# Kernel tuning notes

Hardware: AMD Instinct MI355X
Metric: run time of the kernel (lower is better)

The kernel has to match this reference:

```python
import jax, jax.numpy as jnp
import numpy as np


def setup_inputs() -> dict:
    key = jax.random.key(0)
    kq, kk, kv = jax.random.split(key, 3)
    n, d = 8192, 32
    return {
        "Q": jax.random.normal(kq, (n, d), dtype=jnp.float32),
        "K": jax.random.normal(kk, (n, d), dtype=jnp.float32),
        "V": jax.random.normal(kv, (n, d), dtype=jnp.float32),
    }


def reference(Q, K, V):
    # FlashAttention-2 tiling with online softmax is mathematically equivalent
    # to full (unscaled, unmasked) softmax attention: O = softmax(Q K^T) V.
    # Note: the original module applies NO 1/sqrt(d) scaling.
    S = jnp.einsum("qd,kd->qk", Q, K)           # [n, n]
    P = jax.nn.softmax(S, axis=-1)                # numerically stable softmax
    return jnp.einsum("qk,kd->qd", P, V)         # [n, d]
```

## Files before the change

kernel.cpp:

```cpp
#include <hip/hip_runtime.h>
#include <hip/hip_bf16.h>

typedef __bf16 bf16x8 __attribute__((ext_vector_type(8)));
typedef __bf16 bf16x4 __attribute__((ext_vector_type(4)));
typedef float  f32x4  __attribute__((ext_vector_type(4)));
typedef unsigned short u16;

static constexpr int N = 8192;
static constexpr int D = 32;
static constexpr float L2E = 1.44269504088896340736f;
static constexpr float MSHIFT = 32.0f;

__global__ __launch_bounds__(256) void prep_kernel(
    const float* __restrict__ Q, const float* __restrict__ K,
    const float* __restrict__ V, u16* __restrict__ Qb, u16* __restrict__ Kb,
    u16* __restrict__ Vt) {
  const int b = blockIdx.x;
  auto pack = [](float x, float y) -> unsigned int {
    u16 ux = __builtin_bit_cast(u16, (__bf16)x);
    u16 uy = __builtin_bit_cast(u16, (__bf16)y);
    return (unsigned int)ux | ((unsigned int)uy << 16);
  };
  if (b < 256) {
    const int i = (b * 256 + threadIdx.x) * 4;
    const float4 q = *reinterpret_cast<const float4*>(Q + i);
    const float4 k = *reinterpret_cast<const float4*>(K + i);
    uint2 qo = { pack(q.x * L2E, q.y * L2E), pack(q.z * L2E, q.w * L2E) };
    uint2 ko = { pack(k.x, k.y), pack(k.z, k.w) };
    *reinterpret_cast<uint2*>(Qb + i) = qo;
    *reinterpret_cast<uint2*>(Kb + i) = ko;
  } else {
    const int r = (b - 256) * 256 + threadIdx.x;
    float vr[32];
#pragma unroll
    for (int j = 0; j < 8; ++j) {
      const float4 v = *reinterpret_cast<const float4*>(V + r * D + j * 4);
      vr[4 * j] = v.x; vr[4 * j + 1] = v.y; vr[4 * j + 2] = v.z; vr[4 * j + 3] = v.w;
    }
#pragma unroll
    for (int d = 0; d < 32; ++d)
      Vt[d * N + r] = __builtin_bit_cast(u16, (__bf16)vr[d]);
  }
}

__global__ __launch_bounds__(512, 4) void flash_kernel(
    const u16* __restrict__ Qb, const u16* __restrict__ Kb,
    const u16* __restrict__ Vt, float* __restrict__ lP,
    float* __restrict__ OP, int kpb) {
  __shared__ u16 Ks[2][64 * 32];
  __shared__ u16 Vs[2][32 * 64];

  const int tid = threadIdx.x;
  const int lane = tid & 63;
  const int wave = tid >> 6;
  const int a = lane & 15;
  const int g = lane >> 4;
  const int qg = blockIdx.x & 31;
  const int sp = blockIdx.x >> 5;
  const int qr0 = qg * 256 + wave * 32;
  const int k0 = sp * kpb;
  const int nt = kpb >> 6;

  const bf16x8 qfA = *reinterpret_cast<const bf16x8*>(Qb + (qr0 + a) * D + g * 8);
  const bf16x8 qfB = *reinterpret_cast<const bf16x8*>(Qb + (qr0 + 16 + a) * D + g * 8);

  const int krow = tid >> 3;
  const int ks8 = tid & 7;
  const int kl8 = (((ks8 >> 1) ^ ((krow >> 1) & 3)) << 1) | (ks8 & 1);
  const int vd = tid >> 4;
  const int vps = tid & 15;
  const int vls = vps ^ (vd & 15);
  const u16* __restrict__ ksrc = Kb + krow * D + kl8 * 4;
  const u16* __restrict__ vsrc = Vt + (size_t)vd * N + vls * 4;

  const f32x4 zero4 = {0.f, 0.f, 0.f, 0.f};
  const f32x4 minit = {-MSHIFT, -MSHIFT, -MSHIFT, -MSHIFT};
  f32x4 accA0 = zero4, accA1 = zero4, accB0 = zero4, accB1 = zero4;
  float lA = 0.f, lB = 0.f;

  uint2 kreg = *reinterpret_cast<const uint2*>(ksrc + (size_t)k0 * D);
  uint2 vreg = *reinterpret_cast<const uint2*>(vsrc + k0);
  *reinterpret_cast<uint2*>(&Ks[0][(size_t)tid * 4]) = kreg;
  *reinterpret_cast<uint2*>(&Vs[0][(size_t)tid * 4]) = vreg;
  if (nt > 1) {
    kreg = *reinterpret_cast<const uint2*>(ksrc + (size_t)(k0 + 64) * D);
    vreg = *reinterpret_cast<const uint2*>(vsrc + k0 + 64);
  }
  __syncthreads();

  for (int t = 0; t < nt; ++t) {
    const int cur = t & 1;
    const int nxt = cur ^ 1;
    if (t + 1 < nt) {
      *reinterpret_cast<uint2*>(&Ks[nxt][(size_t)tid * 4]) = kreg;
      *reinterpret_cast<uint2*>(&Vs[nxt][(size_t)tid * 4]) = vreg;
    }
    if (t + 2 < nt) {
      kreg = *reinterpret_cast<const uint2*>(ksrc + (size_t)(k0 + (t + 2) * 64) * D);
      vreg = *reinterpret_cast<const uint2*>(vsrc + k0 + (t + 2) * 64);
    }

    bf16x8 kf[4];
#pragma unroll
    for (int t4 = 0; t4 < 4; ++t4) {
      const int row = 16 * t4 + a;
      kf[t4] = *reinterpret_cast<const bf16x8*>(
          &Ks[cur][row * 32 + ((g ^ ((a >> 1) & 3)) << 3)]);
    }
    bf16x4 v0[4], v1[4];
#pragma unroll
    for (int tt = 0; tt < 4; ++tt) {
      const int slot = ((g + 4 * tt) ^ a) << 2;
      v0[tt] = *reinterpret_cast<const bf16x4*>(&Vs[cur][a * 64 + slot]);
      v1[tt] = *reinterpret_cast<const bf16x4*>(&Vs[cur][(16 + a) * 64 + slot]);
    }

    f32x4 sA[4], sB[4];
#pragma unroll
    for (int t4 = 0; t4 < 4; ++t4) {
      sA[t4] = __builtin_amdgcn_mfma_f32_16x16x32_bf16(kf[t4], qfA, minit, 0, 0, 0);
      sB[t4] = __builtin_amdgcn_mfma_f32_16x16x32_bf16(kf[t4], qfB, minit, 0, 0, 0);
    }

    float pA[4][4], pB[4][4];
#pragma unroll
    for (int t4 = 0; t4 < 4; ++t4) {
#pragma unroll
      for (int r = 0; r < 4; ++r) {
        pA[t4][r] = __builtin_amdgcn_exp2f(sA[t4][r]);
        pB[t4][r] = __builtin_amdgcn_exp2f(sB[t4][r]);
        lA += pA[t4][r];
        lB += pB[t4][r];
      }
    }

    const bf16x8 pfA0 = {(__bf16)pA[0][0], (__bf16)pA[0][1], (__bf16)pA[0][2], (__bf16)pA[0][3],
                         (__bf16)pA[1][0], (__bf16)pA[1][1], (__bf16)pA[1][2], (__bf16)pA[1][3]};
    const bf16x8 pfA1 = {(__bf16)pA[2][0], (__bf16)pA[2][1], (__bf16)pA[2][2], (__bf16)pA[2][3],
                         (__bf16)pA[3][0], (__bf16)pA[3][1], (__bf16)pA[3][2], (__bf16)pA[3][3]};
    const bf16x8 pfB0 = {(__bf16)pB[0][0], (__bf16)pB[0][1], (__bf16)pB[0][2], (__bf16)pB[0][3],
                         (__bf16)pB[1][0], (__bf16)pB[1][1], (__bf16)pB[1][2], (__bf16)pB[1][3]};
    const bf16x8 pfB1 = {(__bf16)pB[2][0], (__bf16)pB[2][1], (__bf16)pB[2][2], (__bf16)pB[2][3],
                         (__bf16)pB[3][0], (__bf16)pB[3][1], (__bf16)pB[3][2], (__bf16)pB[3][3]};

    const bf16x8 va00 = __builtin_shufflevector(v0[0], v0[1], 0, 1, 2, 3, 4, 5, 6, 7);
    const bf16x8 va01 = __builtin_shufflevector(v0[2], v0[3], 0, 1, 2, 3, 4, 5, 6, 7);
    const bf16x8 va10 = __builtin_shufflevector(v1[0], v1[1], 0, 1, 2, 3, 4, 5, 6, 7);
    const bf16x8 va11 = __builtin_shufflevector(v1[2], v1[3], 0, 1, 2, 3, 4, 5, 6, 7);

    accA0 = __builtin_amdgcn_mfma_f32_16x16x32_bf16(va00, pfA0, accA0, 0, 0, 0);
    accA1 = __builtin_amdgcn_mfma_f32_16x16x32_bf16(va10, pfA0, accA1, 0, 0, 0);
    accB0 = __builtin_amdgcn_mfma_f32_16x16x32_bf16(va00, pfB0, accB0, 0, 0, 0);
    accB1 = __builtin_amdgcn_mfma_f32_16x16x32_bf16(va10, pfB0, accB1, 0, 0, 0);
    accA0 = __builtin_amdgcn_mfma_f32_16x16x32_bf16(va01, pfA1, accA0, 0, 0, 0);
    accA1 = __builtin_amdgcn_mfma_f32_16x16x32_bf16(va11, pfA1, accA1, 0, 0, 0);
    accB0 = __builtin_amdgcn_mfma_f32_16x16x32_bf16(va01, pfB1, accB0, 0, 0, 0);
    accB1 = __builtin_amdgcn_mfma_f32_16x16x32_bf16(va11, pfB1, accB1, 0, 0, 0);

    __syncthreads();
  }

  lA += __shfl_xor(lA, 16, 64);
  lA += __shfl_xor(lA, 32, 64);
  lB += __shfl_xor(lB, 16, 64);
  lB += __shfl_xor(lB, 32, 64);

  float* obA = OP + (size_t)(sp * N + qr0 + a) * D;
  float* obB = OP + (size_t)(sp * N + qr0 + 16 + a) * D;
#pragma unroll
  for (int r = 0; r < 4; ++r) {
    obA[4 * g + r] = accA0[r];
    obA[16 + 4 * g + r] = accA1[r];
    obB[4 * g + r] = accB0[r];
    obB[16 + 4 * g + r] = accB1[r];
  }
  if (g == 0) {
    lP[sp * N + qr0 + a] = lA;
    lP[sp * N + qr0 + 16 + a] = lB;
  }
}

template <int NS>
__global__ __launch_bounds__(256) void combine_kernel(
    const float* __restrict__ lP, const float* __restrict__ OP,
    float* __restrict__ out) {
  const int idx = blockIdx.x * 256 + threadIdx.x;
  if (idx >= N * D) return;
  const int q = idx >> 5;
  float L = 0.f, o = 0.f;
#pragma unroll
  for (int s = 0; s < NS; ++s) {
    L += lP[s * N + q];
    o += OP[(size_t)s * N * D + idx];
  }
  out[idx] = o / L;
}

extern "C" void kernel_launch(void* const* d_in, const int* in_sizes, int n_in,
                              void* d_out, int out_size, void* d_ws, size_t ws_size,
                              hipStream_t stream) {
  const float* Q = (const float*)d_in[0];
  const float* K = (const float*)d_in[1];
  const float* V = (const float*)d_in[2];
  float* out = (float*)d_out;

  const size_t base = (size_t)3 * N * D * sizeof(u16);
  const size_t per_split = (size_t)N * sizeof(float) + (size_t)N * D * sizeof(float);
  int ns = 16;
  while (ns > 4 && base + (size_t)ns * per_split > ws_size) ns >>= 1;

  u16* Qb = (u16*)d_ws;
  u16* Kb = Qb + N * D;
  u16* Vt = Kb + N * D;
  float* lP = (float*)(Vt + N * D);
  float* OP = lP + ns * N;

  prep_kernel<<<256 + N / 256, 256, 0, stream>>>(Q, K, V, Qb, Kb, Vt);
  flash_kernel<<<32 * ns, 512, 0, stream>>>(Qb, Kb, Vt, lP, OP, N / ns);
  switch (ns) {
    case 16: combine_kernel<16><<<(N * D) / 256, 256, 0, stream>>>(lP, OP, out); break;
    case 8:  combine_kernel<8><<<(N * D) / 256, 256, 0, stream>>>(lP, OP, out); break;
    default: combine_kernel<4><<<(N * D) / 256, 256, 0, stream>>>(lP, OP, out); break;
  }
}
```

Baseline: 36.03 us.

## Transpose V through LDS and use 128-query blocks with 16-byte tile loads

The V transpose in the prep kernel now stages a 64-row tile in shared memory, so each thread writes a packed 16-byte row of Vt. Previously each thread issued scattered 2-byte global stores. The flash kernel shrinks from 512 to 256 threads per block, covering 128 queries, and launches twice as many blocks. K/V tiles are loaded with 16-byte loads, using a swizzle and half-swap that keep the existing LDS read pattern valid. Scheduling barriers pin the prefetch order; in exchange, each K/V tile is reused by fewer waves, which adds LDS fill traffic per query.

```diff
diff --git a/kernel.cpp b/kernel.cpp
--- a/kernel.cpp
+++ b/kernel.cpp
@@ -15,6 +15,7 @@
     const float* __restrict__ Q, const float* __restrict__ K,
     const float* __restrict__ V, u16* __restrict__ Qb, u16* __restrict__ Kb,
     u16* __restrict__ Vt) {
+  __shared__ float tile[64][33];
   const int b = blockIdx.x;
   auto pack = [](float x, float y) -> unsigned int {
     u16 ux = __builtin_bit_cast(u16, (__bf16)x);
@@ -30,20 +31,28 @@
     *reinterpret_cast<uint2*>(Qb + i) = qo;
     *reinterpret_cast<uint2*>(Kb + i) = ko;
   } else {
-    const int r = (b - 256) * 256 + threadIdx.x;
-    float vr[32];
-#pragma unroll
-    for (int j = 0; j < 8; ++j) {
-      const float4 v = *reinterpret_cast<const float4*>(V + r * D + j * 4);
-      vr[4 * j] = v.x; vr[4 * j + 1] = v.y; vr[4 * j + 2] = v.z; vr[4 * j + 3] = v.w;
-    }
-#pragma unroll
-    for (int d = 0; d < 32; ++d)
-      Vt[d * N + r] = __builtin_bit_cast(u16, (__bf16)vr[d]);
-  }
-}
-
-__global__ __launch_bounds__(512, 4) void flash_kernel(
+    const int r0 = (b - 256) * 64;
+    const int row = threadIdx.x >> 2;
+    const int c0 = (threadIdx.x & 3) * 8;
+    const float4 x0 = *reinterpret_cast<const float4*>(V + (size_t)(r0 + row) * D + c0);
+    const float4 x1 = *reinterpret_cast<const float4*>(V + (size_t)(r0 + row) * D + c0 + 4);
+    tile[row][c0 + 0] = x0.x; tile[row][c0 + 1] = x0.y;
+    tile[row][c0 + 2] = x0.z; tile[row][c0 + 3] = x0.w;
+    tile[row][c0 + 4] = x1.x; tile[row][c0 + 5] = x1.y;
+    tile[row][c0 + 6] = x1.z; tile[row][c0 + 7] = x1.w;
+    __syncthreads();
+    const int d = threadIdx.x >> 3;
+    const int kc = (threadIdx.x & 7) * 8;
+    uint4 o;
+    o.x = pack(tile[kc + 0][d], tile[kc + 1][d]);
+    o.y = pack(tile[kc + 2][d], tile[kc + 3][d]);
+    o.z = pack(tile[kc + 4][d], tile[kc + 5][d]);
+    o.w = pack(tile[kc + 6][d], tile[kc + 7][d]);
+    *reinterpret_cast<uint4*>(Vt + (size_t)d * N + r0 + kc) = o;
+  }
+}
+
+__global__ __launch_bounds__(256, 4) void flash_kernel(
     const u16* __restrict__ Qb, const u16* __restrict__ Kb,
     const u16* __restrict__ Vt, float* __restrict__ lP,
     float* __restrict__ OP, int kpb) {
@@ -55,36 +64,40 @@
   const int wave = tid >> 6;
   const int a = lane & 15;
   const int g = lane >> 4;
-  const int qg = blockIdx.x & 31;
-  const int sp = blockIdx.x >> 5;
-  const int qr0 = qg * 256 + wave * 32;
+  const int qg = blockIdx.x & 63;
+  const int sp = blockIdx.x >> 6;
+  const int qr0 = qg * 128 + wave * 32;
   const int k0 = sp * kpb;
   const int nt = kpb >> 6;
 
   const bf16x8 qfA = *reinterpret_cast<const bf16x8*>(Qb + (qr0 + a) * D + g * 8);
   const bf16x8 qfB = *reinterpret_cast<const bf16x8*>(Qb + (qr0 + 16 + a) * D + g * 8);
 
-  const int krow = tid >> 3;
-  const int ks8 = tid & 7;
-  const int kl8 = (((ks8 >> 1) ^ ((krow >> 1) & 3)) << 1) | (ks8 & 1);
-  const int vd = tid >> 4;
-  const int vps = tid & 15;
-  const int vls = vps ^ (vd & 15);
-  const u16* __restrict__ ksrc = Kb + krow * D + kl8 * 4;
-  const u16* __restrict__ vsrc = Vt + (size_t)vd * N + vls * 4;
-
+  const int krow = tid >> 2;
+  const int kslot = (tid & 3) ^ ((krow >> 1) & 3);
+  const u16* __restrict__ ksrc = Kb + krow * D + kslot * 8;
+  const int vd = tid >> 3;
+  const int v16 = tid & 7;
+  const int vblk = v16 ^ ((vd >> 1) & 7);
+  const bool vswap = (vd & 1) != 0;
+  const u16* __restrict__ vsrc = Vt + (size_t)vd * N + vblk * 8;
+
+  const f32x4 minit = {-MSHIFT, -MSHIFT, -MSHIFT, -MSHIFT};
   const f32x4 zero4 = {0.f, 0.f, 0.f, 0.f};
-  const f32x4 minit = {-MSHIFT, -MSHIFT, -MSHIFT, -MSHIFT};
   f32x4 accA0 = zero4, accA1 = zero4, accB0 = zero4, accB1 = zero4;
   float lA = 0.f, lB = 0.f;
 
-  uint2 kreg = *reinterpret_cast<const uint2*>(ksrc + (size_t)k0 * D);
-  uint2 vreg = *reinterpret_cast<const uint2*>(vsrc + k0);
-  *reinterpret_cast<uint2*>(&Ks[0][(size_t)tid * 4]) = kreg;
-  *reinterpret_cast<uint2*>(&Vs[0][(size_t)tid * 4]) = vreg;
+  {
+    const uint4 kr = *reinterpret_cast<const uint4*>(ksrc + (size_t)k0 * D);
+    const uint4 vr = *reinterpret_cast<const uint4*>(vsrc + k0);
+    const uint4 vw = vswap ? uint4{vr.z, vr.w, vr.x, vr.y} : vr;
+    *reinterpret_cast<uint4*>(&Ks[0][(size_t)tid * 8]) = kr;
+    *reinterpret_cast<uint4*>(&Vs[0][(size_t)tid * 8]) = vw;
+  }
+  uint4 kreg = {0, 0, 0, 0}, vreg = {0, 0, 0, 0};
   if (nt > 1) {
-    kreg = *reinterpret_cast<const uint2*>(ksrc + (size_t)(k0 + 64) * D);
-    vreg = *reinterpret_cast<const uint2*>(vsrc + k0 + 64);
+    kreg = *reinterpret_cast<const uint4*>(ksrc + (size_t)(k0 + 64) * D);
+    vreg = *reinterpret_cast<const uint4*>(vsrc + k0 + 64);
   }
   __syncthreads();
 
@@ -92,13 +105,16 @@
     const int cur = t & 1;
     const int nxt = cur ^ 1;
     if (t + 1 < nt) {
-      *reinterpret_cast<uint2*>(&Ks[nxt][(size_t)tid * 4]) = kreg;
-      *reinterpret_cast<uint2*>(&Vs[nxt][(size_t)tid * 4]) = vreg;
-    }
+      const uint4 vw = vswap ? uint4{vreg.z, vreg.w, vreg.x, vreg.y} : vreg;
+      *reinterpret_cast<uint4*>(&Ks[nxt][(size_t)tid * 8]) = kreg;
+      *reinterpret_cast<uint4*>(&Vs[nxt][(size_t)tid * 8]) = vw;
+    }
+    __builtin_amdgcn_sched_barrier(0);
     if (t + 2 < nt) {
-      kreg = *reinterpret_cast<const uint2*>(ksrc + (size_t)(k0 + (t + 2) * 64) * D);
-      vreg = *reinterpret_cast<const uint2*>(vsrc + k0 + (t + 2) * 64);
-    }
+      kreg = *reinterpret_cast<const uint4*>(ksrc + (size_t)(k0 + (t + 2) * 64) * D);
+      vreg = *reinterpret_cast<const uint4*>(vsrc + k0 + (t + 2) * 64);
+    }
+    __builtin_amdgcn_sched_barrier(0);
 
     bf16x8 kf[4];
 #pragma unroll
@@ -215,8 +231,8 @@
   float* lP = (float*)(Vt + N * D);
   float* OP = lP + ns * N;
 
-  prep_kernel<<<256 + N / 256, 256, 0, stream>>>(Q, K, V, Qb, Kb, Vt);
-  flash_kernel<<<32 * ns, 512, 0, stream>>>(Qb, Kb, Vt, lP, OP, N / ns);
+  prep_kernel<<<256 + N / 64, 256, 0, stream>>>(Q, K, V, Qb, Kb, Vt);
+  flash_kernel<<<64 * ns, 256, 0, stream>>>(Qb, Kb, Vt, lP, OP, N / ns);
   switch (ns) {
     case 16: combine_kernel<16><<<(N * D) / 256, 256, 0, stream>>>(lP, OP, out); break;
     case 8:  combine_kernel<8><<<(N * D) / 256, 256, 0, stream>>>(lP, OP, out); break;
```

Result: faster. 35.16 us (-2.4%).
